# Kernel optimization log

Hardware: AMD Instinct MI355X
Metric: run time of the kernel (lower is better)

Reference implementation:

```python
import jax, jax.numpy as jnp
import numpy as np

B, NINP, NCLS = 16384, 2048, 100


def setup_inputs() -> dict:
    key = jax.random.key(0)
    k1, k2, k3, k4, k5 = jax.random.split(key, 5)
    s = 1.0 / np.sqrt(NINP)
    return {
        "time_series": jax.random.normal(k1, (B, NINP), jnp.float32),
        "w_weight": jax.random.uniform(k2, (NINP, NINP), jnp.float32, -s, s),
        "w_bias": jax.random.uniform(k3, (NINP,), jnp.float32, -s, s),
        "fc_weight": jax.random.uniform(k4, (NCLS, NINP), jnp.float32, -s, s),
        "fc_bias": jax.random.uniform(k5, (NCLS,), jnp.float32, -s, s),
    }


def reference(time_series, w_weight, w_bias, fc_weight, fc_bias):
    # time_series: [B, N]
    n = time_series.shape[1]
    # gamma = cumsum(softmax(w(x), axis=1), axis=1): monotone warp in (0, 1]
    gamma = jnp.cumsum(jax.nn.softmax(time_series @ w_weight.T + w_bias, axis=1), axis=1)
    # Interp1d(linspace(0,1,N), x, gamma): per-row linear interpolation,
    # sampling each series at the warped time points gamma.
    xs = jnp.linspace(0.0, 1.0, n, dtype=time_series.dtype)  # shared knot grid
    warped = jax.vmap(lambda g, y: jnp.interp(g, xs, y))(gamma, time_series)  # [B, N]
    return warped @ fc_weight.T + fc_bias  # [B, nclasses]
```

## Files before the change

kernel.cpp:

```cpp
#include <hip/hip_runtime.h>
#include <hip/hip_bf16.h>

#define BROWS 16384
#define NDIM  2048
#define NCLS  100

typedef __attribute__((ext_vector_type(8))) __bf16 bf16x8;
typedef __attribute__((ext_vector_type(4))) float f32x4;
typedef __attribute__((ext_vector_type(16))) float f32x16;
typedef __attribute__((ext_vector_type(4))) unsigned short u16x4;
typedef __attribute__((ext_vector_type(8))) unsigned short u16x8;

__device__ __forceinline__ unsigned short f2bf(float f) {
    union { float f; unsigned int u; } v; v.f = f;
    unsigned int u = v.u;
    unsigned int r = (u + 0x7fffu + ((u >> 16) & 1u)) >> 16;
    return (unsigned short)r;
}
__device__ __forceinline__ float bf2f(unsigned short h) {
    union { unsigned int u; float f; } v; v.u = ((unsigned int)h) << 16;
    return v.f;
}

#define GLOAD_LDS(g, l) \
    __builtin_amdgcn_global_load_lds((const __attribute__((address_space(1))) void*)(g), \
                                     (__attribute__((address_space(3))) void*)(l), 16, 0, 0)

#define WAITCNT_VM(N) asm volatile("s_waitcnt vmcnt(" #N ")" ::: "memory")
#define RAW_BARRIER() __builtin_amdgcn_s_barrier()

__global__ __launch_bounds__(256) void prep_kernel(const float4* __restrict__ x,
                                                   const float4* __restrict__ w,
                                                   u16x4* __restrict__ xhi, u16x4* __restrict__ xlo,
                                                   u16x4* __restrict__ whi, u16x4* __restrict__ wlo,
                                                   int n4x, int n4w)
{
    int i = blockIdx.x * 256 + threadIdx.x;
    const float4* src; u16x4 *hi, *lo; int idx;
    if (i < n4x) { src = x; hi = xhi; lo = xlo; idx = i; }
    else { idx = i - n4x; if (idx >= n4w) return; src = w; hi = whi; lo = wlo; }
    float4 v = src[idx];
    u16x4 h, l;
    h.x = f2bf(v.x); l.x = f2bf(v.x - bf2f(h.x));
    h.y = f2bf(v.y); l.y = f2bf(v.y - bf2f(h.y));
    h.z = f2bf(v.z); l.z = f2bf(v.z - bf2f(h.z));
    h.w = f2bf(v.w); l.w = f2bf(v.w - bf2f(h.w));
    hi[idx] = h; lo[idx] = l;
}

__global__ __launch_bounds__(256) void cvt_bf16_kernel(const float4* __restrict__ src,
                                                       u16x4* __restrict__ dst, int n4)
{
    int i = blockIdx.x * 256 + threadIdx.x;
    if (i >= n4) return;
    float4 v = src[i];
    u16x4 h;
    h.x = f2bf(v.x); h.y = f2bf(v.y); h.z = f2bf(v.z); h.w = f2bf(v.w);
    dst[i] = h;
}

__global__ __launch_bounds__(512) void gemm1_mfma_fused_kernel(
        const unsigned short* __restrict__ xhi,
        const unsigned short* __restrict__ xlo,
        const unsigned short* __restrict__ whi,
        const unsigned short* __restrict__ wlo,
        const float* __restrict__ bias,
        float* __restrict__ C)
{
    __shared__ unsigned short sAh[3 * 128 * 32];
    __shared__ unsigned short sAl[3 * 128 * 32];
    __shared__ unsigned short sBh[3 * 256 * 32];
    __shared__ unsigned short sBl[3 * 256 * 32];

    const int tid  = threadIdx.x;
    const int lane = tid & 63;
    const int w    = tid >> 6;
    const int wm   = w & 1;
    const int wn   = w >> 1;
    const int m0   = blockIdx.y * 128;
    const int n0   = blockIdx.x * 256;

    const int ra = tid >> 2;
    const int qa = (tid & 3) ^ ((ra >> 1) & 3);
    const size_t a_goff = (size_t)(m0 + ra) * NDIM + qa * 8;
    const int a_lb = (w * 64) * 8;

    size_t b_goff[2]; int b_lb[2];
#pragma unroll
    for (int t = 0; t < 2; t++) {
        const int c = t * 512 + tid;
        const int r = c >> 2;
        const int q = (c & 3) ^ ((r >> 1) & 3);
        b_goff[t] = (size_t)(n0 + r) * NDIM + q * 8;
        b_lb[t]   = (t * 512 + w * 64) * 8;
    }

    const int ln32 = lane & 31;
    const int lk2  = lane >> 5;
    int offA[2][2], offB[2][2];
#pragma unroll
    for (int i = 0; i < 2; i++)
#pragma unroll
        for (int ks = 0; ks < 2; ks++) {
            const int rfa = wm * 64 + i * 32 + ln32;
            offA[i][ks] = rfa * 32 + (((2 * ks + lk2) ^ ((rfa >> 1) & 3)) * 8);
            const int rfb = wn * 64 + i * 32 + ln32;
            offB[i][ks] = rfb * 32 + (((2 * ks + lk2) ^ ((rfb >> 1) & 3)) * 8);
        }

    f32x16 acc[2][2];
#pragma unroll
    for (int i = 0; i < 2; i++)
#pragma unroll
        for (int j = 0; j < 2; j++)
#pragma unroll
            for (int r = 0; r < 16; r++) acc[i][j][r] = 0.f;

#define G1_STAGE(AOFF, BOFF, KT) do { \
    GLOAD_LDS(xhi + a_goff + (KT), &sAh[(AOFF) + a_lb]); \
    GLOAD_LDS(xlo + a_goff + (KT), &sAl[(AOFF) + a_lb]); \
    GLOAD_LDS(whi + b_goff[0] + (KT), &sBh[(BOFF) + b_lb[0]]); \
    GLOAD_LDS(whi + b_goff[1] + (KT), &sBh[(BOFF) + b_lb[1]]); \
    GLOAD_LDS(wlo + b_goff[0] + (KT), &sBl[(BOFF) + b_lb[0]]); \
    GLOAD_LDS(wlo + b_goff[1] + (KT), &sBl[(BOFF) + b_lb[1]]); \
} while (0)

    G1_STAGE(0, 0, 0);
    G1_STAGE(4096, 8192, 32);

    int cA = 0, cB = 0;
    int sA = 2 * 4096, sB = 2 * 8192;

    for (int kt = 0; kt < NDIM; kt += 32) {
        const int skt = (kt + 64 < NDIM) ? kt + 64 : 0;
        G1_STAGE(sA, sB, skt);
        WAITCNT_VM(12);
        RAW_BARRIER();

        __builtin_amdgcn_s_setprio(1);
#pragma unroll
        for (int ks = 0; ks < 2; ks++) {
            bf16x8 ah[2], al[2], bh[2], bl[2];
#pragma unroll
            for (int i = 0; i < 2; i++) {
                ah[i] = *(const bf16x8*)&sAh[cA + offA[i][ks]];
                al[i] = *(const bf16x8*)&sAl[cA + offA[i][ks]];
                bh[i] = *(const bf16x8*)&sBh[cB + offB[i][ks]];
                bl[i] = *(const bf16x8*)&sBl[cB + offB[i][ks]];
            }
#pragma unroll
            for (int i = 0; i < 2; i++)
#pragma unroll
                for (int j = 0; j < 2; j++) {
                    acc[i][j] = __builtin_amdgcn_mfma_f32_32x32x16_bf16(ah[i], bh[j], acc[i][j], 0, 0, 0);
                    acc[i][j] = __builtin_amdgcn_mfma_f32_32x32x16_bf16(ah[i], bl[j], acc[i][j], 0, 0, 0);
                    acc[i][j] = __builtin_amdgcn_mfma_f32_32x32x16_bf16(al[i], bh[j], acc[i][j], 0, 0, 0);
                }
        }
        __builtin_amdgcn_s_setprio(0);
        RAW_BARRIER();

        cA += 4096; if (cA == 12288) cA = 0;
        cB += 8192; if (cB == 24576) cB = 0;
        sA += 4096; if (sA == 12288) sA = 0;
        sB += 8192; if (sB == 24576) sB = 0;
    }

#undef G1_STAGE

    float bb[2];
#pragma unroll
    for (int j = 0; j < 2; j++) bb[j] = bias[n0 + wn * 64 + j * 32 + ln32];
#pragma unroll
    for (int i = 0; i < 2; i++) {
#pragma unroll
        for (int j = 0; j < 2; j++) {
            const int n = n0 + wn * 64 + j * 32 + ln32;
#pragma unroll
            for (int reg = 0; reg < 16; reg++) {
                const int m = m0 + wm * 64 + i * 32 + (reg & 3) + 8 * (reg >> 2) + 4 * lk2;
                C[(size_t)m * NDIM + n] = acc[i][j][reg] + bb[j];
            }
        }
    }
}

#define SXI(i) ((i) + ((i) >> 5))

__global__ __launch_bounds__(256) void warp_bf16_kernel(const unsigned short* __restrict__ Xhi,
                                                        const unsigned short* __restrict__ Xlo,
                                                        const float* __restrict__ L,
                                                        unsigned short* __restrict__ Wout)
{
    const int N = NDIM;
    const int row = blockIdx.x;
    const int tid = threadIdx.x;
    const int lane = tid & 63;
    const int wave = tid >> 6;

    __shared__ float s_x[NDIM + NDIM / 32];
    __shared__ float s_red[4];
    __shared__ float s_wsum[4];

    const float* lrow = L + (size_t)row * N;

    float v[8];
    {
        float4 l0 = *(const float4*)(lrow + tid * 8);
        float4 l1 = *(const float4*)(lrow + tid * 8 + 4);
        v[0] = l0.x; v[1] = l0.y; v[2] = l0.z; v[3] = l0.w;
        v[4] = l1.x; v[5] = l1.y; v[6] = l1.z; v[7] = l1.w;
        u16x8 hx = *(const u16x8*)(Xhi + (size_t)row * N + tid * 8);
        u16x8 lx = *(const u16x8*)(Xlo + (size_t)row * N + tid * 8);
        float xv[8];
#pragma unroll
        for (int j = 0; j < 8; j++) xv[j] = bf2f(hx[j]) + bf2f(lx[j]);
        const int sb = SXI(tid * 8);
        *(float4*)&s_x[sb]     = make_float4(xv[0], xv[1], xv[2], xv[3]);
        *(float4*)&s_x[sb + 4] = make_float4(xv[4], xv[5], xv[6], xv[7]);
    }

    float mx = v[0];
#pragma unroll
    for (int j = 1; j < 8; j++) mx = fmaxf(mx, v[j]);
#pragma unroll
    for (int off = 32; off > 0; off >>= 1) mx = fmaxf(mx, __shfl_down(mx, off));
    if (lane == 0) s_red[wave] = mx;
    __syncthreads();
    mx = fmaxf(fmaxf(s_red[0], s_red[1]), fmaxf(s_red[2], s_red[3]));

    float c = 0.0f;
#pragma unroll
    for (int j = 0; j < 8; j++) {
        float e = __expf(v[j] - mx);
        c += e;
        v[j] = c;
    }

    float sc = c;
#pragma unroll
    for (int off = 1; off < 64; off <<= 1) {
        float t = __shfl_up(sc, off);
        if (lane >= off) sc += t;
    }
    if (lane == 63) s_wsum[wave] = sc;
    __syncthreads();
    float base = 0.0f, total = 0.0f;
#pragma unroll
    for (int w = 0; w < 4; w++) {
        float t = s_wsum[w];
        if (w < wave) base += t;
        total += t;
    }
    const float inv = 1.0f / total;
    const float prefix = base + (sc - c);

    u16x8 o;
#pragma unroll
    for (int j = 0; j < 8; j++) {
        float g = (prefix + v[j]) * inv;
        float pos = g * (float)(N - 1);
        pos = fminf(fmaxf(pos, 0.0f), (float)(N - 1));
        int i = (int)pos;
        if (i > N - 2) i = N - 2;
        float f = pos - (float)i;
        float x0 = s_x[SXI(i)];
        float x1 = s_x[SXI(i + 1)];
        o[j] = f2bf(fmaf(f, x1 - x0, x0));
    }
    *(u16x8*)(Wout + (size_t)row * N + tid * 8) = o;
}

__global__ __launch_bounds__(256) void gemm2_mfma_kernel(
        const unsigned short* __restrict__ Wp,
        const unsigned short* __restrict__ F,
        const float* __restrict__ fb,
        float* __restrict__ out)
{
    __shared__ unsigned short sA[2 * 64 * 64];
    __shared__ unsigned short sB[2 * 128 * 64];

    const int tid  = threadIdx.x;
    const int lane = tid & 63;
    const int w    = tid >> 6;
    const int wm   = w & 1;
    const int wn   = w >> 1;
    const int m0   = blockIdx.x * 64;

    size_t a_goff[2]; int a_lb[2];
#pragma unroll
    for (int t = 0; t < 2; t++) {
        const int c = t * 256 + tid;
        const int r = c >> 3, q = c & 7;
        a_goff[t] = (size_t)(m0 + r) * NDIM + ((q ^ (r & 7)) * 8);
        a_lb[t]   = (t * 256 + w * 64) * 8;
    }
    size_t b_goff[4]; int b_lb[4];
#pragma unroll
    for (int t = 0; t < 4; t++) {
        const int c = t * 256 + tid;
        const int r = c >> 3, q = c & 7;
        b_goff[t] = (size_t)(r < NCLS ? r : NCLS - 1) * NDIM + ((q ^ (r & 7)) * 8);
        b_lb[t]   = (t * 256 + w * 64) * 8;
    }

    const int lm = lane & 15;
    const int lk = lane >> 4;
    int offA[2][2], offB[4][2];
#pragma unroll
    for (int i = 0; i < 2; i++)
#pragma unroll
        for (int ks = 0; ks < 2; ks++) {
            const int r = wm * 32 + i * 16 + lm;
            offA[i][ks] = (r * 8 + ((ks * 4 + lk) ^ (r & 7))) * 8;
        }
#pragma unroll
    for (int j = 0; j < 4; j++)
#pragma unroll
        for (int ks = 0; ks < 2; ks++) {
            const int r = wn * 64 + j * 16 + lm;
            offB[j][ks] = (r * 8 + ((ks * 4 + lk) ^ (r & 7))) * 8;
        }

    f32x4 acc[2][4];
#pragma unroll
    for (int i = 0; i < 2; i++)
#pragma unroll
        for (int j = 0; j < 4; j++) acc[i][j] = (f32x4){0.f, 0.f, 0.f, 0.f};

#define G2_STAGE(B, KT) do { \
    _Pragma("unroll") \
    for (int t = 0; t < 2; t++) GLOAD_LDS(Wp + a_goff[t] + (KT), &sA[(B) * 4096 + a_lb[t]]); \
    _Pragma("unroll") \
    for (int t = 0; t < 4; t++) GLOAD_LDS(F + b_goff[t] + (KT), &sB[(B) * 8192 + b_lb[t]]); \
} while (0)

#define G2_COMPUTE(B) do { \
    _Pragma("unroll") \
    for (int ks = 0; ks < 2; ks++) { \
        bf16x8 af[2], bfr[4]; \
        _Pragma("unroll") \
        for (int i = 0; i < 2; i++) af[i] = *(const bf16x8*)&sA[(B) * 4096 + offA[i][ks]]; \
        _Pragma("unroll") \
        for (int j = 0; j < 4; j++) bfr[j] = *(const bf16x8*)&sB[(B) * 8192 + offB[j][ks]]; \
        _Pragma("unroll") \
        for (int i = 0; i < 2; i++) \
            _Pragma("unroll") \
            for (int j = 0; j < 4; j++) \
                acc[i][j] = __builtin_amdgcn_mfma_f32_16x16x32_bf16(af[i], bfr[j], acc[i][j], 0, 0, 0); \
    } \
} while (0)

    G2_STAGE(0, 0);

    for (int kt = 0; kt < NDIM; kt += 128) {
        G2_STAGE(1, kt + 64);
        WAITCNT_VM(6);
        RAW_BARRIER();
        G2_COMPUTE(0);
        RAW_BARRIER();
        G2_STAGE(0, (kt + 128 < NDIM) ? kt + 128 : 0);
        WAITCNT_VM(6);
        RAW_BARRIER();
        G2_COMPUTE(1);
        RAW_BARRIER();
    }

#undef G2_STAGE
#undef G2_COMPUTE

    const int cn = lane & 15;
    const int rg = lane >> 4;
#pragma unroll
    for (int i = 0; i < 2; i++) {
#pragma unroll
        for (int j = 0; j < 4; j++) {
            const int n = wn * 64 + j * 16 + cn;
            if (n < NCLS) {
                const float bbn = fb[n];
#pragma unroll
                for (int reg = 0; reg < 4; reg++) {
                    const int m = m0 + wm * 32 + i * 16 + rg * 4 + reg;
                    out[(size_t)m * NCLS + n] = acc[i][j][reg] + bbn;
                }
            }
        }
    }
}

__global__ __launch_bounds__(256) void gemm1_kernel(const float* __restrict__ X,
                                                    const float* __restrict__ W,
                                                    const float* __restrict__ bias,
                                                    float* __restrict__ C)
{
    const int K = NDIM;
    __shared__ float sA[16][128];
    __shared__ float sB[16][128];
    const int tid = threadIdx.x;
    const int tx = tid & 15;
    const int ty = tid >> 4;
    const int m0 = blockIdx.y * 128;
    const int n0 = blockIdx.x * 128;
    float acc[8][8];
#pragma unroll
    for (int i = 0; i < 8; i++)
#pragma unroll
        for (int j = 0; j < 8; j++) acc[i][j] = 0.0f;
    const int s_m = tid >> 1;
    const int s_c = (tid & 1) * 8;
    const float* Ag = X + (size_t)(m0 + s_m) * K + s_c;
    const float* Bg = W + (size_t)(n0 + s_m) * K + s_c;
    for (int kt = 0; kt < K; kt += 16) {
        float4 av0 = *(const float4*)(Ag + kt);
        float4 av1 = *(const float4*)(Ag + kt + 4);
        float4 bv0 = *(const float4*)(Bg + kt);
        float4 bv1 = *(const float4*)(Bg + kt + 4);
        __syncthreads();
        sA[s_c + 0][s_m] = av0.x; sA[s_c + 1][s_m] = av0.y;
        sA[s_c + 2][s_m] = av0.z; sA[s_c + 3][s_m] = av0.w;
        sA[s_c + 4][s_m] = av1.x; sA[s_c + 5][s_m] = av1.y;
        sA[s_c + 6][s_m] = av1.z; sA[s_c + 7][s_m] = av1.w;
        sB[s_c + 0][s_m] = bv0.x; sB[s_c + 1][s_m] = bv0.y;
        sB[s_c + 2][s_m] = bv0.z; sB[s_c + 3][s_m] = bv0.w;
        sB[s_c + 4][s_m] = bv1.x; sB[s_c + 5][s_m] = bv1.y;
        sB[s_c + 6][s_m] = bv1.z; sB[s_c + 7][s_m] = bv1.w;
        __syncthreads();
#pragma unroll
        for (int k = 0; k < 16; k++) {
            float4 a0 = *(const float4*)&sA[k][ty * 8];
            float4 a1 = *(const float4*)&sA[k][ty * 8 + 4];
            float4 b0 = *(const float4*)&sB[k][tx * 8];
            float4 b1 = *(const float4*)&sB[k][tx * 8 + 4];
            float a[8] = {a0.x, a0.y, a0.z, a0.w, a1.x, a1.y, a1.z, a1.w};
            float b[8] = {b0.x, b0.y, b0.z, b0.w, b1.x, b1.y, b1.z, b1.w};
#pragma unroll
            for (int i = 0; i < 8; i++)
#pragma unroll
                for (int j = 0; j < 8; j++)
                    acc[i][j] = fmaf(a[i], b[j], acc[i][j]);
        }
    }
    float bb[8];
#pragma unroll
    for (int j = 0; j < 8; j++) bb[j] = bias[n0 + tx * 8 + j];
#pragma unroll
    for (int i = 0; i < 8; i++) {
        const int m = m0 + ty * 8 + i;
        float* crow = C + (size_t)m * NDIM + n0 + tx * 8;
        *(float4*)(crow)     = make_float4(acc[i][0] + bb[0], acc[i][1] + bb[1],
                                           acc[i][2] + bb[2], acc[i][3] + bb[3]);
        *(float4*)(crow + 4) = make_float4(acc[i][4] + bb[4], acc[i][5] + bb[5],
                                           acc[i][6] + bb[6], acc[i][7] + bb[7]);
    }
}

__global__ __launch_bounds__(256) void warp_kernel_f32(const float* __restrict__ X,
                                                       float* __restrict__ L)
{
    const int N = NDIM;
    const int row = blockIdx.x;
    const int tid = threadIdx.x;
    const int lane = tid & 63;
    const int wave = tid >> 6;
    __shared__ float s_x[NDIM];
    __shared__ float s_red[4];
    __shared__ float s_wsum[4];
    float* lrow = L + (size_t)row * N;
    const float* xrow = X + (size_t)row * N;
    float v[8];
    {
        float4 l0 = *(const float4*)(lrow + tid * 8);
        float4 l1 = *(const float4*)(lrow + tid * 8 + 4);
        v[0] = l0.x; v[1] = l0.y; v[2] = l0.z; v[3] = l0.w;
        v[4] = l1.x; v[5] = l1.y; v[6] = l1.z; v[7] = l1.w;
        float4 x0 = *(const float4*)(xrow + tid * 8);
        float4 x1 = *(const float4*)(xrow + tid * 8 + 4);
        *(float4*)&s_x[tid * 8]     = x0;
        *(float4*)&s_x[tid * 8 + 4] = x1;
    }
    float mx = v[0];
#pragma unroll
    for (int j = 1; j < 8; j++) mx = fmaxf(mx, v[j]);
#pragma unroll
    for (int off = 32; off > 0; off >>= 1) mx = fmaxf(mx, __shfl_down(mx, off));
    if (lane == 0) s_red[wave] = mx;
    __syncthreads();
    mx = fmaxf(fmaxf(s_red[0], s_red[1]), fmaxf(s_red[2], s_red[3]));
    float c = 0.0f;
#pragma unroll
    for (int j = 0; j < 8; j++) {
        float e = __expf(v[j] - mx);
        c += e;
        v[j] = c;
    }
    float sc = c;
#pragma unroll
    for (int off = 1; off < 64; off <<= 1) {
        float t = __shfl_up(sc, off);
        if (lane >= off) sc += t;
    }
    if (lane == 63) s_wsum[wave] = sc;
    __syncthreads();
    float base = 0.0f, total = 0.0f;
#pragma unroll
    for (int w = 0; w < 4; w++) {
        float t = s_wsum[w];
        if (w < wave) base += t;
        total += t;
    }
    const float inv = 1.0f / total;
    const float prefix = base + (sc - c);
    float w8[8];
#pragma unroll
    for (int j = 0; j < 8; j++) {
        float g = (prefix + v[j]) * inv;
        float pos = g * (float)(N - 1);
        pos = fminf(fmaxf(pos, 0.0f), (float)(N - 1));
        int i = (int)pos;
        if (i > N - 2) i = N - 2;
        float f = pos - (float)i;
        w8[j] = fmaf(f, s_x[i + 1] - s_x[i], s_x[i]);
    }
    *(float4*)(lrow + tid * 8)     = make_float4(w8[0], w8[1], w8[2], w8[3]);
    *(float4*)(lrow + tid * 8 + 4) = make_float4(w8[4], w8[5], w8[6], w8[7]);
}

__global__ __launch_bounds__(256) void gemm2_kernel(const float* __restrict__ Wp,
                                                    const float* __restrict__ F,
                                                    const float* __restrict__ fb,
                                                    float* __restrict__ out)
{
    const int K = NDIM;
    __shared__ float sA[16][64];
    __shared__ float sB[16][128];
    const int tid = threadIdx.x;
    const int tx = tid & 15;
    const int ty = tid >> 4;
    const int m0 = blockIdx.x * 64;
    float acc[4][8];
#pragma unroll
    for (int i = 0; i < 4; i++)
#pragma unroll
        for (int j = 0; j < 8; j++) acc[i][j] = 0.0f;
    const int a_m = tid >> 2;
    const int a_c = (tid & 3) * 4;
    const int b_n = tid >> 1;
    const int b_c = (tid & 1) * 8;
    const bool bvalid = (b_n < NCLS);
    const float* Ag = Wp + (size_t)(m0 + a_m) * K + a_c;
    const float* Bg = F + (size_t)b_n * K + b_c;
    for (int kt = 0; kt < K; kt += 16) {
        float4 av = *(const float4*)(Ag + kt);
        float4 bv0 = make_float4(0.f, 0.f, 0.f, 0.f);
        float4 bv1 = make_float4(0.f, 0.f, 0.f, 0.f);
        if (bvalid) {
            bv0 = *(const float4*)(Bg + kt);
            bv1 = *(const float4*)(Bg + kt + 4);
        }
        __syncthreads();
        sA[a_c + 0][a_m] = av.x; sA[a_c + 1][a_m] = av.y;
        sA[a_c + 2][a_m] = av.z; sA[a_c + 3][a_m] = av.w;
        sB[b_c + 0][b_n] = bv0.x; sB[b_c + 1][b_n] = bv0.y;
        sB[b_c + 2][b_n] = bv0.z; sB[b_c + 3][b_n] = bv0.w;
        sB[b_c + 4][b_n] = bv1.x; sB[b_c + 5][b_n] = bv1.y;
        sB[b_c + 6][b_n] = bv1.z; sB[b_c + 7][b_n] = bv1.w;
        __syncthreads();
#pragma unroll
        for (int k = 0; k < 16; k++) {
            float4 a4 = *(const float4*)&sA[k][ty * 4];
            float4 b0 = *(const float4*)&sB[k][tx * 8];
            float4 b1 = *(const float4*)&sB[k][tx * 8 + 4];
            float a[4] = {a4.x, a4.y, a4.z, a4.w};
            float b[8] = {b0.x, b0.y, b0.z, b0.w, b1.x, b1.y, b1.z, b1.w};
#pragma unroll
            for (int i = 0; i < 4; i++)
#pragma unroll
                for (int j = 0; j < 8; j++)
                    acc[i][j] = fmaf(a[i], b[j], acc[i][j]);
        }
    }
#pragma unroll
    for (int i = 0; i < 4; i++) {
        const int m = m0 + ty * 4 + i;
#pragma unroll
        for (int j = 0; j < 8; j++) {
            const int n = tx * 8 + j;
            if (n < NCLS) out[(size_t)m * NCLS + n] = acc[i][j] + fb[n];
        }
    }
}

extern "C" void kernel_launch(void* const* d_in, const int* in_sizes, int n_in,
                              void* d_out, int out_size, void* d_ws, size_t ws_size,
                              hipStream_t stream) {
    const float* x  = (const float*)d_in[0];
    const float* ww = (const float*)d_in[1];
    const float* wb = (const float*)d_in[2];
    const float* fw = (const float*)d_in[3];
    const float* fb = (const float*)d_in[4];
    float* out = (float*)d_out;

    char* ws = (char*)d_ws;
    float* logits = (float*)ws;
    const size_t LOGITS_B = (size_t)BROWS * NDIM * 4;
    const size_t XBF_B    = (size_t)BROWS * NDIM * 2;
    const size_t WBF_B    = (size_t)NDIM * NDIM * 2;
    unsigned short* xhi = (unsigned short*)(ws + LOGITS_B);
    unsigned short* xlo = (unsigned short*)(ws + LOGITS_B + XBF_B);
    unsigned short* whi = (unsigned short*)(ws + LOGITS_B + 2 * XBF_B);
    unsigned short* wlo = (unsigned short*)(ws + LOGITS_B + 2 * XBF_B + WBF_B);
    unsigned short* wbf = xlo;
    unsigned short* fwb = wlo;
    const size_t WS_NEED = LOGITS_B + 2 * XBF_B + 2 * WBF_B;

    if (ws_size >= WS_NEED) {
        const int n4x = BROWS * NDIM / 4;
        const int n4w = NDIM * NDIM / 4;
        prep_kernel<<<(n4x + n4w + 255) / 256, 256, 0, stream>>>(
            (const float4*)x, (const float4*)ww,
            (u16x4*)xhi, (u16x4*)xlo, (u16x4*)whi, (u16x4*)wlo, n4x, n4w);
        gemm1_mfma_fused_kernel<<<dim3(NDIM / 256, BROWS / 128), 512, 0, stream>>>(
            xhi, xlo, whi, wlo, wb, logits);
        warp_bf16_kernel<<<BROWS, 256, 0, stream>>>(xhi, xlo, logits, wbf);
        cvt_bf16_kernel<<<(NCLS * NDIM / 4 + 255) / 256, 256, 0, stream>>>(
            (const float4*)fw, (u16x4*)fwb, NCLS * NDIM / 4);
        gemm2_mfma_kernel<<<BROWS / 64, 256, 0, stream>>>(wbf, fwb, fb, out);
    } else {
        gemm1_kernel<<<dim3(NDIM / 128, BROWS / 128), 256, 0, stream>>>(x, ww, wb, logits);
        warp_kernel_f32<<<BROWS, 256, 0, stream>>>(x, logits);
        gemm2_kernel<<<BROWS / 64, 256, 0, stream>>>(logits, fw, fb, out);
    }
}
```

Measured before the change: 752.8 us.

## Interleave gemm1 prefetch with split k-steps; halve gemm2 row tile

The gemm1 main loop is split into two half-steps. Each half issues its LDS fragment reads, then part of the next stage's global-to-LDS loads, then waits on lgkmcnt before its MFMAs, so memory traffic and LDS reads overlap compute more finely. gemm2 now uses 32-row tiles with each of four waves covering 32 classes across the whole M tile, which doubles the grid size for better occupancy. The price is more barriers per k-step and more redundant reads of the classifier weights.

After: 664.9 us, median of 2. 11.7% less time.

```diff
diff --git a/kernel.cpp b/kernel.cpp
--- a/kernel.cpp
+++ b/kernel.cpp
@@ -27,6 +27,10 @@
                                      (__attribute__((address_space(3))) void*)(l), 16, 0, 0)
 
 #define WAITCNT_VM(N) asm volatile("s_waitcnt vmcnt(" #N ")" ::: "memory")
+#define WAITCNT_LGKM0() do { \
+    asm volatile("s_waitcnt lgkmcnt(0)" ::: "memory"); \
+    __builtin_amdgcn_sched_barrier(0); \
+} while (0)
 #define RAW_BARRIER() __builtin_amdgcn_s_barrier()
 
 __global__ __launch_bounds__(256) void prep_kernel(const float4* __restrict__ x,
@@ -116,7 +120,7 @@
 #pragma unroll
             for (int r = 0; r < 16; r++) acc[i][j][r] = 0.f;
 
-#define G1_STAGE(AOFF, BOFF, KT) do { \
+#define G1_STAGE_ALL(AOFF, BOFF, KT) do { \
     GLOAD_LDS(xhi + a_goff + (KT), &sAh[(AOFF) + a_lb]); \
     GLOAD_LDS(xlo + a_goff + (KT), &sAl[(AOFF) + a_lb]); \
     GLOAD_LDS(whi + b_goff[0] + (KT), &sBh[(BOFF) + b_lb[0]]); \
@@ -125,29 +129,32 @@
     GLOAD_LDS(wlo + b_goff[1] + (KT), &sBl[(BOFF) + b_lb[1]]); \
 } while (0)
 
-    G1_STAGE(0, 0, 0);
-    G1_STAGE(4096, 8192, 32);
+    G1_STAGE_ALL(0, 0, 0);
+    G1_STAGE_ALL(4096, 8192, 32);
+    WAITCNT_VM(6);
+    RAW_BARRIER();
 
     int cA = 0, cB = 0;
     int sA = 2 * 4096, sB = 2 * 8192;
 
     for (int kt = 0; kt < NDIM; kt += 32) {
         const int skt = (kt + 64 < NDIM) ? kt + 64 : 0;
-        G1_STAGE(sA, sB, skt);
-        WAITCNT_VM(12);
-        RAW_BARRIER();
-
-        __builtin_amdgcn_s_setprio(1);
-#pragma unroll
-        for (int ks = 0; ks < 2; ks++) {
+
+        {
             bf16x8 ah[2], al[2], bh[2], bl[2];
 #pragma unroll
             for (int i = 0; i < 2; i++) {
-                ah[i] = *(const bf16x8*)&sAh[cA + offA[i][ks]];
-                al[i] = *(const bf16x8*)&sAl[cA + offA[i][ks]];
-                bh[i] = *(const bf16x8*)&sBh[cB + offB[i][ks]];
-                bl[i] = *(const bf16x8*)&sBl[cB + offB[i][ks]];
+                ah[i] = *(const bf16x8*)&sAh[cA + offA[i][0]];
+                al[i] = *(const bf16x8*)&sAl[cA + offA[i][0]];
+                bh[i] = *(const bf16x8*)&sBh[cB + offB[i][0]];
+                bl[i] = *(const bf16x8*)&sBl[cB + offB[i][0]];
             }
+            GLOAD_LDS(xhi + a_goff + skt, &sAh[sA + a_lb]);
+            GLOAD_LDS(xlo + a_goff + skt, &sAl[sA + a_lb]);
+            GLOAD_LDS(whi + b_goff[0] + skt, &sBh[sB + b_lb[0]]);
+            RAW_BARRIER();
+            WAITCNT_LGKM0();
+            __builtin_amdgcn_s_setprio(1);
 #pragma unroll
             for (int i = 0; i < 2; i++)
 #pragma unroll
@@ -156,9 +163,37 @@
                     acc[i][j] = __builtin_amdgcn_mfma_f32_32x32x16_bf16(ah[i], bl[j], acc[i][j], 0, 0, 0);
                     acc[i][j] = __builtin_amdgcn_mfma_f32_32x32x16_bf16(al[i], bh[j], acc[i][j], 0, 0, 0);
                 }
-        }
-        __builtin_amdgcn_s_setprio(0);
-        RAW_BARRIER();
+            __builtin_amdgcn_s_setprio(0);
+            RAW_BARRIER();
+        }
+
+        {
+            bf16x8 ah[2], al[2], bh[2], bl[2];
+#pragma unroll
+            for (int i = 0; i < 2; i++) {
+                ah[i] = *(const bf16x8*)&sAh[cA + offA[i][1]];
+                al[i] = *(const bf16x8*)&sAl[cA + offA[i][1]];
+                bh[i] = *(const bf16x8*)&sBh[cB + offB[i][1]];
+                bl[i] = *(const bf16x8*)&sBl[cB + offB[i][1]];
+            }
+            GLOAD_LDS(whi + b_goff[1] + skt, &sBh[sB + b_lb[1]]);
+            GLOAD_LDS(wlo + b_goff[0] + skt, &sBl[sB + b_lb[0]]);
+            GLOAD_LDS(wlo + b_goff[1] + skt, &sBl[sB + b_lb[1]]);
+            WAITCNT_VM(6);
+            RAW_BARRIER();
+            WAITCNT_LGKM0();
+            __builtin_amdgcn_s_setprio(1);
+#pragma unroll
+            for (int i = 0; i < 2; i++)
+#pragma unroll
+                for (int j = 0; j < 2; j++) {
+                    acc[i][j] = __builtin_amdgcn_mfma_f32_32x32x16_bf16(ah[i], bh[j], acc[i][j], 0, 0, 0);
+                    acc[i][j] = __builtin_amdgcn_mfma_f32_32x32x16_bf16(ah[i], bl[j], acc[i][j], 0, 0, 0);
+                    acc[i][j] = __builtin_amdgcn_mfma_f32_32x32x16_bf16(al[i], bh[j], acc[i][j], 0, 0, 0);
+                }
+            __builtin_amdgcn_s_setprio(0);
+            RAW_BARRIER();
+        }
 
         cA += 4096; if (cA == 12288) cA = 0;
         cB += 8192; if (cB == 24576) cB = 0;
@@ -166,7 +201,7 @@
         sB += 8192; if (sB == 24576) sB = 0;
     }
 
-#undef G1_STAGE
+#undef G1_STAGE_ALL
 
     float bb[2];
 #pragma unroll
@@ -277,24 +312,18 @@
         const float* __restrict__ fb,
         float* __restrict__ out)
 {
-    __shared__ unsigned short sA[2 * 64 * 64];
+    __shared__ unsigned short sA[2 * 32 * 64];
     __shared__ unsigned short sB[2 * 128 * 64];
 
     const int tid  = threadIdx.x;
     const int lane = tid & 63;
     const int w    = tid >> 6;
-    const int wm   = w & 1;
-    const int wn   = w >> 1;
-    const int m0   = blockIdx.x * 64;
-
-    size_t a_goff[2]; int a_lb[2];
-#pragma unroll
-    for (int t = 0; t < 2; t++) {
-        const int c = t * 256 + tid;
-        const int r = c >> 3, q = c & 7;
-        a_goff[t] = (size_t)(m0 + r) * NDIM + ((q ^ (r & 7)) * 8);
-        a_lb[t]   = (t * 256 + w * 64) * 8;
-    }
+    const int m0   = blockIdx.x * 32;
+
+    const int ar = tid >> 3, aq = tid & 7;
+    const size_t a_goff = (size_t)(m0 + ar) * NDIM + ((aq ^ (ar & 7)) * 8);
+    const int a_lb = (w * 64) * 8;
+
     size_t b_goff[4]; int b_lb[4];
 #pragma unroll
     for (int t = 0; t < 4; t++) {
@@ -306,31 +335,25 @@
 
     const int lm = lane & 15;
     const int lk = lane >> 4;
-    int offA[2][2], offB[4][2];
+    int offA[2][2], offB[2][2];
 #pragma unroll
     for (int i = 0; i < 2; i++)
 #pragma unroll
         for (int ks = 0; ks < 2; ks++) {
-            const int r = wm * 32 + i * 16 + lm;
+            const int r = i * 16 + lm;
             offA[i][ks] = (r * 8 + ((ks * 4 + lk) ^ (r & 7))) * 8;
-        }
-#pragma unroll
-    for (int j = 0; j < 4; j++)
-#pragma unroll
-        for (int ks = 0; ks < 2; ks++) {
-            const int r = wn * 64 + j * 16 + lm;
-            offB[j][ks] = (r * 8 + ((ks * 4 + lk) ^ (r & 7))) * 8;
-        }
-
-    f32x4 acc[2][4];
+            const int rb = w * 32 + i * 16 + lm;
+            offB[i][ks] = (rb * 8 + ((ks * 4 + lk) ^ (rb & 7))) * 8;
+        }
+
+    f32x4 acc[2][2];
 #pragma unroll
     for (int i = 0; i < 2; i++)
 #pragma unroll
-        for (int j = 0; j < 4; j++) acc[i][j] = (f32x4){0.f, 0.f, 0.f, 0.f};
+        for (int j = 0; j < 2; j++) acc[i][j] = (f32x4){0.f, 0.f, 0.f, 0.f};
 
 #define G2_STAGE(B, KT) do { \
-    _Pragma("unroll") \
-    for (int t = 0; t < 2; t++) GLOAD_LDS(Wp + a_goff[t] + (KT), &sA[(B) * 4096 + a_lb[t]]); \
+    GLOAD_LDS(Wp + a_goff + (KT), &sA[(B) * 2048 + a_lb]); \
     _Pragma("unroll") \
     for (int t = 0; t < 4; t++) GLOAD_LDS(F + b_goff[t] + (KT), &sB[(B) * 8192 + b_lb[t]]); \
 } while (0)
@@ -338,15 +361,16 @@
 #define G2_COMPUTE(B) do { \
     _Pragma("unroll") \
     for (int ks = 0; ks < 2; ks++) { \
-        bf16x8 af[2], bfr[4]; \
+        bf16x8 af[2], bfr[2]; \
         _Pragma("unroll") \
-        for (int i = 0; i < 2; i++) af[i] = *(const bf16x8*)&sA[(B) * 4096 + offA[i][ks]]; \
-        _Pragma("unroll") \
-        for (int j = 0; j < 4; j++) bfr[j] = *(const bf16x8*)&sB[(B) * 8192 + offB[j][ks]]; \
+        for (int i = 0; i < 2; i++) { \
+            af[i]  = *(const bf16x8*)&sA[(B) * 2048 + offA[i][ks]]; \
+            bfr[i] = *(const bf16x8*)&sB[(B) * 8192 + offB[i][ks]]; \
+        } \
         _Pragma("unroll") \
         for (int i = 0; i < 2; i++) \
             _Pragma("unroll") \
-            for (int j = 0; j < 4; j++) \
+            for (int j = 0; j < 2; j++) \
                 acc[i][j] = __builtin_amdgcn_mfma_f32_16x16x32_bf16(af[i], bfr[j], acc[i][j], 0, 0, 0); \
     } \
 } while (0)
@@ -355,12 +379,12 @@
 
     for (int kt = 0; kt < NDIM; kt += 128) {
         G2_STAGE(1, kt + 64);
-        WAITCNT_VM(6);
+        WAITCNT_VM(5);
         RAW_BARRIER();
         G2_COMPUTE(0);
         RAW_BARRIER();
         G2_STAGE(0, (kt + 128 < NDIM) ? kt + 128 : 0);
-        WAITCNT_VM(6);
+        WAITCNT_VM(5);
         RAW_BARRIER();
         G2_COMPUTE(1);
         RAW_BARRIER();
@@ -374,13 +398,13 @@
 #pragma unroll
     for (int i = 0; i < 2; i++) {
 #pragma unroll
-        for (int j = 0; j < 4; j++) {
-            const int n = wn * 64 + j * 16 + cn;
+        for (int j = 0; j < 2; j++) {
+            const int n = w * 32 + j * 16 + cn;
             if (n < NCLS) {
                 const float bbn = fb[n];
 #pragma unroll
                 for (int reg = 0; reg < 4; reg++) {
-                    const int m = m0 + wm * 32 + i * 16 + rg * 4 + reg;
+                    const int m = m0 + i * 16 + rg * 4 + reg;
                     out[(size_t)m * NCLS + n] = acc[i][j][reg] + bbn;
                 }
             }
@@ -624,7 +648,7 @@
         warp_bf16_kernel<<<BROWS, 256, 0, stream>>>(xhi, xlo, logits, wbf);
         cvt_bf16_kernel<<<(NCLS * NDIM / 4 + 255) / 256, 256, 0, stream>>>(
             (const float4*)fw, (u16x4*)fwb, NCLS * NDIM / 4);
-        gemm2_mfma_kernel<<<BROWS / 64, 256, 0, stream>>>(wbf, fwb, fb, out);
+        gemm2_mfma_kernel<<<BROWS / 32, 256, 0, stream>>>(wbf, fwb, fb, out);
     } else {
         gemm1_kernel<<<dim3(NDIM / 128, BROWS / 128), 256, 0, stream>>>(x, ww, wb, logits);
         warp_kernel_f32<<<BROWS, 256, 0, stream>>>(x, logits);
```
